# Kernel tuning notes

Measured on AMD Instinct MI355X. Metric: run time of the kernel, lower is better.

Reference implementation:

```python
import jax, jax.numpy as jnp
import numpy as np

TAU = 2.0
V_TH = 1.0


def setup_inputs() -> dict:
    key = jax.random.key(0)
    k1, k2, k3 = jax.random.split(key, 3)
    T, B, H = 128, 64, 1024
    x = jax.random.normal(k1, (T, B, H), dtype=jnp.float32)
    # nn.Linear(H, H, bias=False) weights, shape [out, in]
    W1 = jax.random.normal(k2, (H, H), dtype=jnp.float32) / np.sqrt(H)
    W2 = jax.random.normal(k3, (H, H), dtype=jnp.float32) / np.sqrt(H)
    return {"x": x, "W1": W1, "W2": W2}


def _lif_scan(x_proj):
    # x_proj: [T, B, H]; membrane v starts at 0.
    def step(v, xt):
        h = v + (xt - v) / TAU          # leaky integrate
        s = (h >= V_TH).astype(h.dtype)  # hard-threshold spike
        v_new = h * (1.0 - s)            # soft reset (to 0 on spike)
        return v_new, s

    v0 = jnp.zeros(x_proj.shape[1:], dtype=x_proj.dtype)
    _, spikes = jax.lax.scan(step, v0, x_proj)
    return spikes  # [T, B, H]


def reference(x, W1, W2):
    # fc1 applied per timestep == one batched GEMM over [T*B, H]
    x_proj = jnp.einsum('tbh,oh->tbo', x, W1)
    spike = _lif_scan(x_proj)
    out = jnp.einsum('tbh,oh->tbo', spike, W2)
    return out
```

## Files before the change

### kernel.cpp

```cpp
#include <hip/hip_runtime.h>
#include <hip/hip_bf16.h>
#include <stdint.h>

#define TT 128
#define BB 64
#define HH 1024
#define MM (TT * BB)
#define NLANE (BB * HH)
#define DELTA 1.0e-4
#define F16_ONE 0x3C00

typedef __attribute__((ext_vector_type(8))) short bf16x8;
typedef __attribute__((ext_vector_type(8))) _Float16 f16x8;
typedef __attribute__((ext_vector_type(4))) float f32x4;

#define GLOAD16(g, l)                                                        \
    __builtin_amdgcn_global_load_lds(                                        \
        (const __attribute__((address_space(1))) unsigned int*)(g),          \
        (__attribute__((address_space(3))) unsigned int*)(l), 16, 0, 0)

#define FENCE() __builtin_amdgcn_sched_barrier(0)

static __device__ __forceinline__ unsigned short bf16_bits(float f) {
    __hip_bfloat16 b = __float2bfloat16(f);
    return *reinterpret_cast<unsigned short*>(&b);
}
static __device__ __forceinline__ unsigned short f16_bits(float f) {
    _Float16 h = (_Float16)f;
    return *reinterpret_cast<unsigned short*>(&h);
}

__global__ __launch_bounds__(256) void prep_fused(const float* __restrict__ x,
                                                  const float* __restrict__ W1,
                                                  const float* __restrict__ W2,
                                                  unsigned short* __restrict__ A2,
                                                  unsigned short* __restrict__ B2,
                                                  unsigned short* __restrict__ w2h,
                                                  int* __restrict__ cnt) {
    const int bid = blockIdx.x;
    if (bid == 0 && threadIdx.x == 0) *cnt = 0;

    if (bid < 9216) {
        const bool isX = (bid < 8192);
        const int i = (isX ? bid : bid - 8192) * 256 + threadIdx.x;
        const float4 v4 = reinterpret_cast<const float4*>(isX ? x : W1)[i];
        float v[4] = {v4.x, v4.y, v4.z, v4.w};
        unsigned short hb[4], lb[4];
#pragma unroll
        for (int c = 0; c < 4; c++) {
            hb[c] = bf16_bits(v[c]);
            __hip_bfloat16 hh = *reinterpret_cast<__hip_bfloat16*>(&hb[c]);
            lb[c] = bf16_bits(v[c] - __bfloat162float(hh));
        }
        ushort4* dst = reinterpret_cast<ushort4*>(isX ? A2 : B2);
        const int r = i >> 8;
        const int c4 = i & 255;
        dst[(size_t)r * 512 + c4]       = make_ushort4(hb[0], hb[1], hb[2], hb[3]);
        dst[(size_t)r * 512 + 256 + c4] = make_ushort4(lb[0], lb[1], lb[2], lb[3]);
    } else {
        const int i = (bid - 9216) * 256 + threadIdx.x;
        const float4 v4 = reinterpret_cast<const float4*>(W2)[i];
        float v[4] = {v4.x, v4.y, v4.z, v4.w};
        unsigned short hb[4];
#pragma unroll
        for (int c = 0; c < 4; c++) hb[c] = f16_bits(v[c]);
        reinterpret_cast<ushort4*>(w2h)[i] = make_ushort4(hb[0], hb[1], hb[2], hb[3]);
    }
}

__global__ __launch_bounds__(512, 2) void gemm1_tb(const unsigned short* __restrict__ A2,
                                                   const unsigned short* __restrict__ B2,
                                                   float* __restrict__ C) {
    __shared__ short As_[3][256 * 64];
    __shared__ short Bs_[3][128 * 64];

    const int tid = threadIdx.x;
    const int lane = tid & 63;
    const int wave = tid >> 6;
    const int wr = wave >> 1;
    const int wc = wave & 1;

    const int bid = blockIdx.x;
    const int orig = (bid & 7) * 32 + (bid >> 3);
    const int m0 = (orig >> 3) * 256;
    const int n0 = (orig & 7) * 128;

    const int rsel = lane & 15;
    const int part = lane >> 4;

    int adrA[4][2], adrB[4][2];
#pragma unroll
    for (int mi = 0; mi < 4; mi++) {
        const int ra = wr * 64 + mi * 16 + rsel;
#pragma unroll
        for (int ks = 0; ks < 2; ks++) {
            const int slot = ks * 4 + part;
            adrA[mi][ks] = ra * 64 + ((slot ^ (ra & 7)) << 3);
        }
    }
#pragma unroll
    for (int ni = 0; ni < 4; ni++) {
        const int rb = wc * 64 + ni * 16 + rsel;
#pragma unroll
        for (int ks = 0; ks < 2; ks++) {
            const int slot = ks * 4 + part;
            adrB[ni][ks] = rb * 64 + ((slot ^ (rb & 7)) << 3);
        }
    }

    const int srow = tid >> 3;
    const int gslot8 = ((tid & 7) ^ (srow & 7)) << 3;
    const int ldso = wave * 512;

#define STAGE_A(buf, q, kcol)                                                     \
    GLOAD16(&A2[(size_t)(m0 + (q) * 64 + srow) * 2048 + (kcol) + gslot8],         \
            &As_[buf][(q) * 4096 + ldso])
#define STAGE_B(buf, b, kcol)                                                     \
    GLOAD16(&B2[(size_t)(n0 + (b) * 64 + srow) * 2048 + (kcol) + gslot8],         \
            &Bs_[buf][(b) * 4096 + ldso])

#define KA_OF(t) (((t) < 16) ? (t) * 64 : (t) * 64 - 1024)
#define KB_OF(t) (((t) < 32) ? (t) * 64 : (t) * 64 - 2048)

    STAGE_A(0, 0, 0); STAGE_A(0, 1, 0); STAGE_A(0, 2, 0); STAGE_A(0, 3, 0);
    STAGE_B(0, 0, 0); STAGE_B(0, 1, 0);
    STAGE_A(1, 0, 64); STAGE_A(1, 1, 64); STAGE_A(1, 2, 64); STAGE_A(1, 3, 64);
    STAGE_B(1, 0, 64); STAGE_B(1, 1, 64);
    asm volatile("s_waitcnt vmcnt(6)" ::: "memory");
    FENCE();
    __builtin_amdgcn_s_barrier();
    FENCE();

    f32x4 acc[4][4] = {};
    int bufr = 0;

    for (int t = 0; t < 48; ++t) {
        const short* As = As_[bufr];
        const short* Bs = Bs_[bufr];
        int sbuf = bufr + 2; if (sbuf >= 3) sbuf -= 3;
        const int tc = (t + 2 < 48) ? t + 2 : 47;
        const int kA2 = KA_OF(tc);
        const int kB2 = KB_OF(tc);

        bf16x8 a[4], b[4];

#pragma unroll
        for (int mi = 0; mi < 4; mi++)
            a[mi] = *reinterpret_cast<const bf16x8*>(&As[adrA[mi][0]]);
#pragma unroll
        for (int ni = 0; ni < 4; ni++)
            b[ni] = *reinterpret_cast<const bf16x8*>(&Bs[adrB[ni][0]]);
        STAGE_A(sbuf, 0, kA2);
        STAGE_A(sbuf, 1, kA2);
        STAGE_B(sbuf, 0, kB2);
        __builtin_amdgcn_s_setprio(1);
#pragma unroll
        for (int mi = 0; mi < 4; mi++)
#pragma unroll
            for (int ni = 0; ni < 4; ni++)
                acc[mi][ni] = __builtin_amdgcn_mfma_f32_16x16x32_bf16(a[mi], b[ni], acc[mi][ni], 0, 0, 0);
        __builtin_amdgcn_s_setprio(0);

#pragma unroll
        for (int mi = 0; mi < 4; mi++)
            a[mi] = *reinterpret_cast<const bf16x8*>(&As[adrA[mi][1]]);
#pragma unroll
        for (int ni = 0; ni < 4; ni++)
            b[ni] = *reinterpret_cast<const bf16x8*>(&Bs[adrB[ni][1]]);
        STAGE_A(sbuf, 2, kA2);
        STAGE_A(sbuf, 3, kA2);
        STAGE_B(sbuf, 1, kB2);
        __builtin_amdgcn_s_setprio(1);
#pragma unroll
        for (int mi = 0; mi < 4; mi++)
#pragma unroll
            for (int ni = 0; ni < 4; ni++)
                acc[mi][ni] = __builtin_amdgcn_mfma_f32_16x16x32_bf16(a[mi], b[ni], acc[mi][ni], 0, 0, 0);
        __builtin_amdgcn_s_setprio(0);

        asm volatile("s_waitcnt vmcnt(6)" ::: "memory");
        FENCE();
        __builtin_amdgcn_s_barrier();
        FENCE();

        bufr = (bufr == 2) ? 0 : bufr + 1;
    }
#undef STAGE_A
#undef STAGE_B

    asm volatile("s_waitcnt vmcnt(0)" ::: "memory");

    const int col = lane & 15;
    const int quad = lane >> 4;
#pragma unroll
    for (int mi = 0; mi < 4; mi++)
#pragma unroll
        for (int ni = 0; ni < 4; ni++) {
            const int m = m0 + wr * 64 + mi * 16 + quad * 4;
            const int n = n0 + wc * 64 + ni * 16 + col;
            float* dst = &C[(size_t)m * HH + n];
#pragma unroll
            for (int r = 0; r < 4; r++)
                dst[(size_t)r * HH] = acc[mi][ni][r];
        }
}

__global__ __launch_bounds__(256) void lif_scan_flag(const float* __restrict__ xp,
                                                     unsigned short* __restrict__ sp,
                                                     int* __restrict__ count,
                                                     int* __restrict__ list) {
    const int idx = blockIdx.x * 256 + threadIdx.x;
    double v = 0.0;
    bool flg = false;
#pragma unroll 4
    for (int t = 0; t < TT; t++) {
        const double x = (double)xp[(size_t)t * NLANE + idx];
        const double h = v + (x - v) * 0.5;
        const bool s = (h >= 1.0);
        flg |= (fabs(h - 1.0) < DELTA);
        v = s ? 0.0 : h;
        sp[(size_t)t * NLANE + idx] = s ? (unsigned short)F16_ONE : (unsigned short)0;
    }
    if (flg) {
        const int i = atomicAdd(count, 1);
        list[i] = idx;
    }
}

__global__ __launch_bounds__(1024) void recompute_fused(const float* __restrict__ X,
                                                        const float* __restrict__ W1,
                                                        const int* __restrict__ count,
                                                        const int* __restrict__ list,
                                                        unsigned short* __restrict__ sp) {
    __shared__ double hbuf[TT];
    const int cnt = *count;
    const int wv = threadIdx.x >> 6;
    const int ln = threadIdx.x & 63;

    for (int li = blockIdx.x; li < cnt; li += gridDim.x) {
        const int lane = list[li];
        const int b = lane >> 10;
        const int h = lane & (HH - 1);
        const float4* w4 = reinterpret_cast<const float4*>(W1 + (size_t)h * HH);

        for (int t = wv; t < TT; t += 16) {
            const float4* x4 = reinterpret_cast<const float4*>(X + (size_t)(t * BB + b) * HH);
            double s0 = 0.0, s1 = 0.0, s2 = 0.0, s3 = 0.0;
#pragma unroll
            for (int i = 0; i < 4; i++) {
                const float4 xa = x4[ln + i * 64];
                const float4 wa = w4[ln + i * 64];
                s0 = fma((double)xa.x, (double)wa.x, s0);
                s1 = fma((double)xa.y, (double)wa.y, s1);
                s2 = fma((double)xa.z, (double)wa.z, s2);
                s3 = fma((double)xa.w, (double)wa.w, s3);
            }
            double s = (s0 + s1) + (s2 + s3);
#pragma unroll
            for (int off = 32; off >= 1; off >>= 1)
                s += __shfl_down(s, off);
            if (ln == 0) hbuf[t] = s;
        }
        __syncthreads();

        if (threadIdx.x == 0) {
            double v = 0.0;
            for (int t = 0; t < TT; t++) {
                const double hh = v + (hbuf[t] - v) * 0.5;
                const bool s = (hh >= 1.0);
                v = s ? 0.0 : hh;
                sp[(size_t)t * NLANE + lane] = s ? (unsigned short)F16_ONE : (unsigned short)0;
            }
        }
        __syncthreads();
    }
}

__global__ __launch_bounds__(256) void gemm2_mfma(const unsigned short* __restrict__ S,
                                                  const unsigned short* __restrict__ W,
                                                  float* __restrict__ O) {
    __shared__ short As[128 * 32];
    __shared__ short Bs[64 * 32];

    const int tid = threadIdx.x;
    const int lane = tid & 63;
    const int wave = tid >> 6;
    const int m0 = blockIdx.y * 128;
    const int n0 = blockIdx.x * 64;
    const int wm = (wave >> 1) * 64;
    const int wn = (wave & 1) * 32;

    const int rsel = lane & 15;
    const int part = lane >> 4;

    int adrA[4], adrB[2];
#pragma unroll
    for (int i = 0; i < 4; i++) {
        const int ra = wm + i * 16 + rsel;
        adrA[i] = ra * 32 + (part ^ ((ra >> 1) & 3)) * 8;
    }
#pragma unroll
    for (int i = 0; i < 2; i++) {
        const int rb = wn + i * 16 + rsel;
        adrB[i] = rb * 32 + (part ^ ((rb >> 1) & 3)) * 8;
    }

    f32x4 acc[4][2] = {};

    for (int k0 = 0; k0 < HH; k0 += 32) {
#pragma unroll
        for (int p = 0; p < 3; p++) {
            const int c = tid + p * 256;
            const int cb = wave * 64 + p * 256;
            if (c < 512) {
                const int row = c >> 2;
                const int pslot = c & 3;
                const int pdata = pslot ^ ((row >> 1) & 3);
                GLOAD16(&S[(size_t)(m0 + row) * HH + k0 + pdata * 8], &As[cb * 8]);
            } else {
                const int c2 = c - 512;
                const int row = c2 >> 2;
                const int pslot = c2 & 3;
                const int pdata = pslot ^ ((row >> 1) & 3);
                GLOAD16(&W[(size_t)(n0 + row) * HH + k0 + pdata * 8], &Bs[(cb - 512) * 8]);
            }
        }
        __syncthreads();

        f16x8 a[4], b[2];
#pragma unroll
        for (int mi = 0; mi < 4; mi++)
            a[mi] = *reinterpret_cast<f16x8*>(&As[adrA[mi]]);
#pragma unroll
        for (int ni = 0; ni < 2; ni++)
            b[ni] = *reinterpret_cast<f16x8*>(&Bs[adrB[ni]]);

#pragma unroll
        for (int mi = 0; mi < 4; mi++)
#pragma unroll
            for (int ni = 0; ni < 2; ni++)
                acc[mi][ni] = __builtin_amdgcn_mfma_f32_16x16x32_f16(
                    a[mi], b[ni], acc[mi][ni], 0, 0, 0);

        __syncthreads();
    }

    const int col = lane & 15;
    const int quad = lane >> 4;
#pragma unroll
    for (int mi = 0; mi < 4; mi++)
#pragma unroll
        for (int ni = 0; ni < 2; ni++) {
            const int m = m0 + wm + mi * 16 + quad * 4;
            const int n = n0 + wn + ni * 16 + col;
            float* dst = &O[(size_t)m * HH + n];
#pragma unroll
            for (int r = 0; r < 4; r++)
                dst[(size_t)r * HH] = acc[mi][ni][r];
        }
}

extern "C" void kernel_launch(void* const* d_in, const int* in_sizes, int n_in,
                              void* d_out, int out_size, void* d_ws, size_t ws_size,
                              hipStream_t stream) {
    const float* x  = (const float*)d_in[0];
    const float* W1 = (const float*)d_in[1];
    const float* W2 = (const float*)d_in[2];
    float* out = (float*)d_out;

    char* ws = (char*)d_ws;

    unsigned short* A2   = (unsigned short*)ws;
    unsigned short* B2   = A2 + (size_t)MM * 2048;
    unsigned short* w2h  = B2 + (size_t)HH * 2048;
    int*            list = (int*)(w2h + (size_t)HH * HH);
    int*            cnt  = list + NLANE;
    float*          xp   = (float*)(((uintptr_t)(cnt + 64) + 255) & ~(uintptr_t)255);
    unsigned short* sp   = (unsigned short*)ws;

    prep_fused<<<10240, 256, 0, stream>>>(x, W1, W2, A2, B2, w2h, cnt);

    gemm1_tb<<<256, 512, 0, stream>>>(A2, B2, xp);

    lif_scan_flag<<<NLANE / 256, 256, 0, stream>>>(xp, sp, cnt, list);

    recompute_fused<<<512, 1024, 0, stream>>>(x, W1, cnt, list, sp);

    dim3 g2(HH / 64, MM / 128);
    gemm2_mfma<<<g2, 256, 0, stream>>>(sp, w2h, out);
}
```

Measured before the change: 214.6 us.

## Load GEMM1 B operand directly into registers, bypassing LDS staging

The B tile of gemm1 is no longer staged through shared memory. Each wave now issues inline-asm global_load_dwordx4 straight into double-buffered register fragments, prefetched one k-step ahead. The A tile keeps its triple-buffered LDS pipeline, and the loop is restructured to two tiles per iteration with a single barrier each and a larger vmcnt window. This aims to cut LDS traffic and capacity use, at the cost of more VGPR pressure and redundant global reads of B across waves that share the same columns.

New measurement: 268.7 us. 25.2% more time.

```diff
diff --git a/kernel.cpp b/kernel.cpp
--- a/kernel.cpp
+++ b/kernel.cpp
@@ -68,11 +68,10 @@
     }
 }
 
-__global__ __launch_bounds__(512, 2) void gemm1_tb(const unsigned short* __restrict__ A2,
-                                                   const unsigned short* __restrict__ B2,
-                                                   float* __restrict__ C) {
+__global__ __launch_bounds__(512, 2) void gemm1_breg(const unsigned short* __restrict__ A2,
+                                                     const unsigned short* __restrict__ B2,
+                                                     float* __restrict__ C) {
     __shared__ short As_[3][256 * 64];
-    __shared__ short Bs_[3][128 * 64];
 
     const int tid = threadIdx.x;
     const int lane = tid & 63;
@@ -88,7 +87,7 @@
     const int rsel = lane & 15;
     const int part = lane >> 4;
 
-    int adrA[4][2], adrB[4][2];
+    int adrA[4][2];
 #pragma unroll
     for (int mi = 0; mi < 4; mi++) {
         const int ra = wr * 64 + mi * 16 + rsel;
@@ -98,15 +97,6 @@
             adrA[mi][ks] = ra * 64 + ((slot ^ (ra & 7)) << 3);
         }
     }
-#pragma unroll
-    for (int ni = 0; ni < 4; ni++) {
-        const int rb = wc * 64 + ni * 16 + rsel;
-#pragma unroll
-        for (int ks = 0; ks < 2; ks++) {
-            const int slot = ks * 4 + part;
-            adrB[ni][ks] = rb * 64 + ((slot ^ (rb & 7)) << 3);
-        }
-    }
 
     const int srow = tid >> 3;
     const int gslot8 = ((tid & 7) ^ (srow & 7)) << 3;
@@ -115,80 +105,90 @@
 #define STAGE_A(buf, q, kcol)                                                     \
     GLOAD16(&A2[(size_t)(m0 + (q) * 64 + srow) * 2048 + (kcol) + gslot8],         \
             &As_[buf][(q) * 4096 + ldso])
-#define STAGE_B(buf, b, kcol)                                                     \
-    GLOAD16(&B2[(size_t)(n0 + (b) * 64 + srow) * 2048 + (kcol) + gslot8],         \
-            &Bs_[buf][(b) * 4096 + ldso])
+
+    const unsigned short* sbase = B2 + (size_t)n0 * 2048;
+    int voffNi[4];
+    {
+        const int vbase = (((wc * 64 + rsel) * 2048) + part * 8) * 2;
+#pragma unroll
+        for (int ni = 0; ni < 4; ni++) voffNi[ni] = vbase + ni * 65536;
+    }
+
+#define LOADB(S, kb2)                                                             \
+    do {                                                                          \
+        int _v0 = voffNi[0] + (kb2);                                              \
+        int _v1 = voffNi[1] + (kb2);                                              \
+        int _v2 = voffNi[2] + (kb2);                                              \
+        int _v3 = voffNi[3] + (kb2);                                              \
+        asm volatile("global_load_dwordx4 %0, %1, %2 offset:0"  : "=&v"(S[0][0]) : "v"(_v0), "s"(sbase)); \
+        asm volatile("global_load_dwordx4 %0, %1, %2 offset:64" : "=&v"(S[0][1]) : "v"(_v0), "s"(sbase)); \
+        asm volatile("global_load_dwordx4 %0, %1, %2 offset:0"  : "=&v"(S[1][0]) : "v"(_v1), "s"(sbase)); \
+        asm volatile("global_load_dwordx4 %0, %1, %2 offset:64" : "=&v"(S[1][1]) : "v"(_v1), "s"(sbase)); \
+        asm volatile("global_load_dwordx4 %0, %1, %2 offset:0"  : "=&v"(S[2][0]) : "v"(_v2), "s"(sbase)); \
+        asm volatile("global_load_dwordx4 %0, %1, %2 offset:64" : "=&v"(S[2][1]) : "v"(_v2), "s"(sbase)); \
+        asm volatile("global_load_dwordx4 %0, %1, %2 offset:0"  : "=&v"(S[3][0]) : "v"(_v3), "s"(sbase)); \
+        asm volatile("global_load_dwordx4 %0, %1, %2 offset:64" : "=&v"(S[3][1]) : "v"(_v3), "s"(sbase)); \
+    } while (0)
 
 #define KA_OF(t) (((t) < 16) ? (t) * 64 : (t) * 64 - 1024)
 #define KB_OF(t) (((t) < 32) ? (t) * 64 : (t) * 64 - 2048)
 
+    bf16x8 bs0[4][2], bs1[4][2];
+    f32x4 acc[4][4] = {};
+
     STAGE_A(0, 0, 0); STAGE_A(0, 1, 0); STAGE_A(0, 2, 0); STAGE_A(0, 3, 0);
-    STAGE_B(0, 0, 0); STAGE_B(0, 1, 0);
+    LOADB(bs0, 0);
     STAGE_A(1, 0, 64); STAGE_A(1, 1, 64); STAGE_A(1, 2, 64); STAGE_A(1, 3, 64);
-    STAGE_B(1, 0, 64); STAGE_B(1, 1, 64);
-    asm volatile("s_waitcnt vmcnt(6)" ::: "memory");
+    asm volatile("s_waitcnt vmcnt(12)" ::: "memory");
     FENCE();
     __builtin_amdgcn_s_barrier();
     FENCE();
 
-    f32x4 acc[4][4] = {};
-    int bufr = 0;
-
-    for (int t = 0; t < 48; ++t) {
-        const short* As = As_[bufr];
-        const short* Bs = Bs_[bufr];
-        int sbuf = bufr + 2; if (sbuf >= 3) sbuf -= 3;
-        const int tc = (t + 2 < 48) ? t + 2 : 47;
-        const int kA2 = KA_OF(tc);
-        const int kB2 = KB_OF(tc);
-
-        bf16x8 a[4], b[4];
-
-#pragma unroll
-        for (int mi = 0; mi < 4; mi++)
-            a[mi] = *reinterpret_cast<const bf16x8*>(&As[adrA[mi][0]]);
-#pragma unroll
-        for (int ni = 0; ni < 4; ni++)
-            b[ni] = *reinterpret_cast<const bf16x8*>(&Bs[adrB[ni][0]]);
-        STAGE_A(sbuf, 0, kA2);
-        STAGE_A(sbuf, 1, kA2);
-        STAGE_B(sbuf, 0, kB2);
-        __builtin_amdgcn_s_setprio(1);
-#pragma unroll
-        for (int mi = 0; mi < 4; mi++)
-#pragma unroll
-            for (int ni = 0; ni < 4; ni++)
-                acc[mi][ni] = __builtin_amdgcn_mfma_f32_16x16x32_bf16(a[mi], b[ni], acc[mi][ni], 0, 0, 0);
-        __builtin_amdgcn_s_setprio(0);
-
-#pragma unroll
-        for (int mi = 0; mi < 4; mi++)
-            a[mi] = *reinterpret_cast<const bf16x8*>(&As[adrA[mi][1]]);
-#pragma unroll
-        for (int ni = 0; ni < 4; ni++)
-            b[ni] = *reinterpret_cast<const bf16x8*>(&Bs[adrB[ni][1]]);
-        STAGE_A(sbuf, 2, kA2);
-        STAGE_A(sbuf, 3, kA2);
-        STAGE_B(sbuf, 1, kB2);
-        __builtin_amdgcn_s_setprio(1);
-#pragma unroll
-        for (int mi = 0; mi < 4; mi++)
-#pragma unroll
-            for (int ni = 0; ni < 4; ni++)
-                acc[mi][ni] = __builtin_amdgcn_mfma_f32_16x16x32_bf16(a[mi], b[ni], acc[mi][ni], 0, 0, 0);
-        __builtin_amdgcn_s_setprio(0);
-
-        asm volatile("s_waitcnt vmcnt(6)" ::: "memory");
-        FENCE();
-        __builtin_amdgcn_s_barrier();
-        FENCE();
-
-        bufr = (bufr == 2) ? 0 : bufr + 1;
-    }
+#define TILE(t_, SU, SL)                                                          \
+    do {                                                                          \
+        const int t = (t_);                                                       \
+        const short* As = As_[t % 3];                                             \
+        const int sbuf = (t + 2) % 3;                                             \
+        const int tc = (t + 2 < 48) ? t + 2 : 47;     \
+        const int kA2 = KA_OF(tc);                                                \
+        const int tb = (t + 1 < 48) ? t + 1 : 47;                                 \
+        const int kB1 = KB_OF(tb) * 2;                                            \
+        bf16x8 a[4][2];                                                           \
+        _Pragma("unroll")                                                         \
+        for (int mi = 0; mi < 4; mi++) {                                          \
+            a[mi][0] = *reinterpret_cast<const bf16x8*>(&As[adrA[mi][0]]);        \
+            a[mi][1] = *reinterpret_cast<const bf16x8*>(&As[adrA[mi][1]]);        \
+        }                                                                         \
+        STAGE_A(sbuf, 0, kA2); STAGE_A(sbuf, 1, kA2);                             \
+        STAGE_A(sbuf, 2, kA2); STAGE_A(sbuf, 3, kA2);                             \
+        LOADB(SL, kB1);                                                           \
+        asm volatile("s_waitcnt vmcnt(12)" ::: "memory");    \
+        FENCE();                                                                  \
+        __builtin_amdgcn_s_barrier();                                             \
+        FENCE();                                                                  \
+        __builtin_amdgcn_s_setprio(1);                                            \
+        _Pragma("unroll")                                                         \
+        for (int mi = 0; mi < 4; mi++)                                            \
+            _Pragma("unroll")                                                     \
+            for (int ni = 0; ni < 4; ni++) {                                      \
+                acc[mi][ni] = __builtin_amdgcn_mfma_f32_16x16x32_bf16(            \
+                    a[mi][0], SU[ni][0], acc[mi][ni], 0, 0, 0);                   \
+                acc[mi][ni] = __builtin_amdgcn_mfma_f32_16x16x32_bf16(            \
+                    a[mi][1], SU[ni][1], acc[mi][ni], 0, 0, 0);                   \
+            }                                                                     \
+        __builtin_amdgcn_s_setprio(0);                                            \
+    } while (0)
+
+    for (int tp = 0; tp < 24; ++tp) {
+        TILE(tp * 2,     bs0, bs1);
+        TILE(tp * 2 + 1, bs1, bs0);
+    }
+#undef TILE
 #undef STAGE_A
-#undef STAGE_B
+#undef LOADB
 
     asm volatile("s_waitcnt vmcnt(0)" ::: "memory");
+    FENCE();
 
     const int col = lane & 15;
     const int quad = lane >> 4;
@@ -380,7 +380,7 @@
 
     prep_fused<<<10240, 256, 0, stream>>>(x, W1, W2, A2, B2, w2h, cnt);
 
-    gemm1_tb<<<256, 512, 0, stream>>>(A2, B2, xp);
+    gemm1_breg<<<256, 512, 0, stream>>>(A2, B2, xp);
 
     lif_scan_flag<<<NLANE / 256, 256, 0, stream>>>(xp, sp, cnt, list);
 
```

## Restructure split-bf16 GEMM1 to 4 waves with 128-row tiles and shared hi/lo fragments

Applied to the files above, without the earlier changes.

GEMM1 now runs 256-thread blocks of 4 waves, each computing a 128x64 sub-tile, instead of 8 waves with 64x64 sub-tiles. The K loop now walks 32 steps over hi/lo column pairs. Each step loads the hi and lo A/B fragments once and issues three MFMA passes (hi*hi, hi*lo, lo*hi) from registers, instead of treating the concatenated hi/lo K dimension as 48 separate steps. The goal is more MFMA work per LDS read and per barrier and fewer redundant fragment loads. In exchange the kernel uses more accumulator registers, has fewer waves per block, and uses a new swizzled staging layout.

After: 221.1 us. +3.1%, slower.

```diff
diff --git a/kernel.cpp b/kernel.cpp
--- a/kernel.cpp
+++ b/kernel.cpp
@@ -68,9 +68,9 @@
     }
 }
 
-__global__ __launch_bounds__(512, 2) void gemm1_tb(const unsigned short* __restrict__ A2,
-                                                   const unsigned short* __restrict__ B2,
-                                                   float* __restrict__ C) {
+__global__ __launch_bounds__(256, 1) void gemm1_w128(const unsigned short* __restrict__ A2,
+                                                     const unsigned short* __restrict__ B2,
+                                                     float* __restrict__ C) {
     __shared__ short As_[3][256 * 64];
     __shared__ short Bs_[3][128 * 64];
 
@@ -88,115 +88,119 @@
     const int rsel = lane & 15;
     const int part = lane >> 4;
 
-    int adrA[4][2], adrB[4][2];
-#pragma unroll
-    for (int mi = 0; mi < 4; mi++) {
-        const int ra = wr * 64 + mi * 16 + rsel;
-#pragma unroll
-        for (int ks = 0; ks < 2; ks++) {
-            const int slot = ks * 4 + part;
-            adrA[mi][ks] = ra * 64 + ((slot ^ (ra & 7)) << 3);
-        }
+    int adrA[8], adrB[4];
+#pragma unroll
+    for (int mi = 0; mi < 8; mi++) {
+        const int ra = wr * 128 + mi * 16 + rsel;
+        adrA[mi] = ra * 64 + ((part ^ (ra & 7)) << 3);
     }
 #pragma unroll
     for (int ni = 0; ni < 4; ni++) {
         const int rb = wc * 64 + ni * 16 + rsel;
-#pragma unroll
-        for (int ks = 0; ks < 2; ks++) {
-            const int slot = ks * 4 + part;
-            adrB[ni][ks] = rb * 64 + ((slot ^ (rb & 7)) << 3);
-        }
+        adrB[ni] = rb * 64 + ((part ^ (rb & 7)) << 3);
     }
 
     const int srow = tid >> 3;
-    const int gslot8 = ((tid & 7) ^ (srow & 7)) << 3;
+    const int lsw  = (tid & 7) ^ (srow & 7);
+    const int src_sw = (lsw & 3) * 8 + (lsw >> 2) * 1024;
     const int ldso = wave * 512;
 
-#define STAGE_A(buf, q, kcol)                                                     \
-    GLOAD16(&A2[(size_t)(m0 + (q) * 64 + srow) * 2048 + (kcol) + gslot8],         \
-            &As_[buf][(q) * 4096 + ldso])
-#define STAGE_B(buf, b, kcol)                                                     \
-    GLOAD16(&B2[(size_t)(n0 + (b) * 64 + srow) * 2048 + (kcol) + gslot8],         \
-            &Bs_[buf][(b) * 4096 + ldso])
-
-#define KA_OF(t) (((t) < 16) ? (t) * 64 : (t) * 64 - 1024)
-#define KB_OF(t) (((t) < 32) ? (t) * 64 : (t) * 64 - 2048)
-
-    STAGE_A(0, 0, 0); STAGE_A(0, 1, 0); STAGE_A(0, 2, 0); STAGE_A(0, 3, 0);
-    STAGE_B(0, 0, 0); STAGE_B(0, 1, 0);
-    STAGE_A(1, 0, 64); STAGE_A(1, 1, 64); STAGE_A(1, 2, 64); STAGE_A(1, 3, 64);
-    STAGE_B(1, 0, 64); STAGE_B(1, 1, 64);
-    asm volatile("s_waitcnt vmcnt(6)" ::: "memory");
+#define STAGE_A(buf, q, kc)                                                       \
+    GLOAD16(&A2[(size_t)(m0 + (q) * 32 + srow) * 2048 + (kc) + src_sw],           \
+            &As_[buf][(q) * 2048 + ldso])
+#define STAGE_B(buf, b, kc)                                                       \
+    GLOAD16(&B2[(size_t)(n0 + (b) * 32 + srow) * 2048 + (kc) + src_sw],           \
+            &Bs_[buf][(b) * 2048 + ldso])
+#define STAGE_G1(buf, kc)  do { STAGE_A(buf,0,kc); STAGE_A(buf,1,kc); STAGE_A(buf,2,kc); STAGE_A(buf,3,kc); } while (0)
+#define STAGE_G2(buf, kc)  do { STAGE_A(buf,4,kc); STAGE_A(buf,5,kc); STAGE_A(buf,6,kc); STAGE_A(buf,7,kc); } while (0)
+#define STAGE_G3(buf, kc)  do { STAGE_B(buf,0,kc); STAGE_B(buf,1,kc); STAGE_B(buf,2,kc); STAGE_B(buf,3,kc); } while (0)
+
+    f32x4 acc[8][4] = {};
+
+    STAGE_G1(0, 0); STAGE_G2(0, 0); STAGE_G3(0, 0);
+    STAGE_G1(1, 32); STAGE_G2(1, 32); STAGE_G3(1, 32);
+    asm volatile("s_waitcnt vmcnt(12)" ::: "memory");
     FENCE();
     __builtin_amdgcn_s_barrier();
     FENCE();
 
-    f32x4 acc[4][4] = {};
     int bufr = 0;
 
-    for (int t = 0; t < 48; ++t) {
+    for (int t = 0; t < 32; ++t) {
         const short* As = As_[bufr];
         const short* Bs = Bs_[bufr];
-        int sbuf = bufr + 2; if (sbuf >= 3) sbuf -= 3;
-        const int tc = (t + 2 < 48) ? t + 2 : 47;
-        const int kA2 = KA_OF(tc);
-        const int kB2 = KB_OF(tc);
-
-        bf16x8 a[4], b[4];
-
-#pragma unroll
-        for (int mi = 0; mi < 4; mi++)
-            a[mi] = *reinterpret_cast<const bf16x8*>(&As[adrA[mi][0]]);
+        const int bstg = (bufr + 2 >= 3) ? bufr - 1 : bufr + 2;
+        const int tc = (t + 2 < 32) ? t + 2 : 31;
+        const int kc2 = tc * 32;
+
+        bf16x8 aH[8], aL[8], bH[4], bL[4];
+
+        aH[0] = *reinterpret_cast<const bf16x8*>(&As[adrA[0]]);
 #pragma unroll
         for (int ni = 0; ni < 4; ni++)
-            b[ni] = *reinterpret_cast<const bf16x8*>(&Bs[adrB[ni][0]]);
-        STAGE_A(sbuf, 0, kA2);
-        STAGE_A(sbuf, 1, kA2);
-        STAGE_B(sbuf, 0, kB2);
-        __builtin_amdgcn_s_setprio(1);
-#pragma unroll
-        for (int mi = 0; mi < 4; mi++)
+            bH[ni] = *reinterpret_cast<const bf16x8*>(&Bs[adrB[ni]]);
+#pragma unroll
+        for (int mi = 1; mi < 8; mi++)
+            aH[mi] = *reinterpret_cast<const bf16x8*>(&As[adrA[mi]]);
+        FENCE();
+        STAGE_G1(bstg, kc2);
+        FENCE();
+
+#pragma unroll
+        for (int mi = 0; mi < 8; mi++)
 #pragma unroll
             for (int ni = 0; ni < 4; ni++)
-                acc[mi][ni] = __builtin_amdgcn_mfma_f32_16x16x32_bf16(a[mi], b[ni], acc[mi][ni], 0, 0, 0);
-        __builtin_amdgcn_s_setprio(0);
-
-#pragma unroll
-        for (int mi = 0; mi < 4; mi++)
-            a[mi] = *reinterpret_cast<const bf16x8*>(&As[adrA[mi][1]]);
+                acc[mi][ni] = __builtin_amdgcn_mfma_f32_16x16x32_bf16(aH[mi], bH[ni], acc[mi][ni], 0, 0, 0);
+        FENCE();
+
 #pragma unroll
         for (int ni = 0; ni < 4; ni++)
-            b[ni] = *reinterpret_cast<const bf16x8*>(&Bs[adrB[ni][1]]);
-        STAGE_A(sbuf, 2, kA2);
-        STAGE_A(sbuf, 3, kA2);
-        STAGE_B(sbuf, 1, kB2);
-        __builtin_amdgcn_s_setprio(1);
-#pragma unroll
-        for (int mi = 0; mi < 4; mi++)
+            bL[ni] = *reinterpret_cast<const bf16x8*>(&Bs[adrB[ni] ^ 32]);
+#pragma unroll
+        for (int mi = 0; mi < 8; mi++)
+            aL[mi] = *reinterpret_cast<const bf16x8*>(&As[adrA[mi] ^ 32]);
+        FENCE();
+        STAGE_G2(bstg, kc2);
+        STAGE_G3(bstg, kc2);
+        FENCE();
+
+#pragma unroll
+        for (int mi = 0; mi < 8; mi++)
 #pragma unroll
             for (int ni = 0; ni < 4; ni++)
-                acc[mi][ni] = __builtin_amdgcn_mfma_f32_16x16x32_bf16(a[mi], b[ni], acc[mi][ni], 0, 0, 0);
-        __builtin_amdgcn_s_setprio(0);
-
-        asm volatile("s_waitcnt vmcnt(6)" ::: "memory");
+                acc[mi][ni] = __builtin_amdgcn_mfma_f32_16x16x32_bf16(aH[mi], bL[ni], acc[mi][ni], 0, 0, 0);
+        FENCE();
+
+#pragma unroll
+        for (int mi = 0; mi < 8; mi++)
+#pragma unroll
+            for (int ni = 0; ni < 4; ni++)
+                acc[mi][ni] = __builtin_amdgcn_mfma_f32_16x16x32_bf16(aL[mi], bH[ni], acc[mi][ni], 0, 0, 0);
+        FENCE();
+
+        asm volatile("s_waitcnt vmcnt(12) lgkmcnt(0)" ::: "memory");
         FENCE();
         __builtin_amdgcn_s_barrier();
         FENCE();
 
         bufr = (bufr == 2) ? 0 : bufr + 1;
     }
+#undef STAGE_G1
+#undef STAGE_G2
+#undef STAGE_G3
 #undef STAGE_A
 #undef STAGE_B
 
-    asm volatile("s_waitcnt vmcnt(0)" ::: "memory");
+    asm volatile("s_waitcnt vmcnt(0) lgkmcnt(0)" ::: "memory");
+    FENCE();
 
     const int col = lane & 15;
     const int quad = lane >> 4;
 #pragma unroll
-    for (int mi = 0; mi < 4; mi++)
+    for (int mi = 0; mi < 8; mi++)
 #pragma unroll
         for (int ni = 0; ni < 4; ni++) {
-            const int m = m0 + wr * 64 + mi * 16 + quad * 4;
+            const int m = m0 + wr * 128 + mi * 16 + quad * 4;
             const int n = n0 + wc * 64 + ni * 16 + col;
             float* dst = &C[(size_t)m * HH + n];
 #pragma unroll
@@ -380,7 +384,7 @@
 
     prep_fused<<<10240, 256, 0, stream>>>(x, W1, W2, A2, B2, w2h, cnt);
 
-    gemm1_tb<<<256, 512, 0, stream>>>(A2, B2, xp);
+    gemm1_w128<<<256, 256, 0, stream>>>(A2, B2, xp);
 
     lif_scan_flag<<<NLANE / 256, 256, 0, stream>>>(xp, sp, cnt, list);
 
```
